# Kernel tuning notes

Measured on AMD Instinct MI355X. Metric: run time of the kernel, lower is better.

Reference implementation:

```python
import jax, jax.numpy as jnp
import numpy as np

GAMMA = 0.96875
HIDDEN = 512


def setup_inputs() -> dict:
    key = jax.random.key(0)
    kx, kq, kk, kv = jax.random.split(key, 4)
    B, S, H = 8, 2048, HIDDEN
    X = jax.random.normal(kx, (B, S, H), dtype=jnp.float32)
    # matches torch.randn(H, H) / H initialization
    W_Q = jax.random.normal(kq, (H, H), dtype=jnp.float32) / H
    W_K = jax.random.normal(kk, (H, H), dtype=jnp.float32) / H
    W_V = jax.random.normal(kv, (H, H), dtype=jnp.float32) / H  # v_dim == hidden (double_v_dim=False)
    return {"X": X, "W_Q": W_Q, "W_K": W_K, "W_V": W_V}


def reference(X, W_Q, W_K, W_V):
    # X: [B, S, H]
    Q = X @ W_Q  # [B, S, H]
    K = X @ W_K  # [B, S, H]
    V = X @ W_V  # [B, S, H]
    S_len = X.shape[1]
    idx = jnp.arange(S_len)
    D = GAMMA ** jnp.abs(idx[None, :] - idx[:, None]).astype(X.dtype)  # [S, S]
    scores = jnp.einsum('bsh,bth->bst', Q, K) * D  # [B, S, S]
    # swish(x) = x * sigmoid(x)
    ret = jnp.einsum('bst,bth->bsh', scores * jax.nn.sigmoid(scores), V)
    return ret
```

## Files before the change

### kernel.cpp

```cpp
#include <hip/hip_runtime.h>


typedef short  bf16x8 __attribute__((ext_vector_type(8)));
typedef float  f32x4  __attribute__((ext_vector_type(4)));

constexpr int S_LEN = 2048;
constexpr int HID   = 512;
constexpr int BAND  = 256;

#define GAMMA_L2 (-0.045803689613125f)
#define LOG2E    (1.4426950408889634f)

__device__ __forceinline__ ushort f2bf(float f) {
  union { float f; unsigned u; } v; v.f = f;
  unsigned u = v.u;
  u += 0x7FFFu + ((u >> 16) & 1u);
  return (ushort)(u >> 16);
}

__device__ __forceinline__ void gld_lds16(const ushort* g, ushort* l) {
  __builtin_amdgcn_global_load_lds(
      (const __attribute__((address_space(1))) void*)g,
      (__attribute__((address_space(3))) void*)l, 16, 0, 0);
}

__global__ void cvt_x_kernel(const float* __restrict__ X, ushort* __restrict__ Xb) {
  const int n4 = (8 * S_LEN * HID) / 4;
  int i = blockIdx.x * blockDim.x + threadIdx.x;
  const int stride = gridDim.x * blockDim.x;
  for (; i < n4; i += stride) {
    float4 v = ((const float4*)X)[i];
    ushort4 o;
    o.x = f2bf(v.x); o.y = f2bf(v.y); o.z = f2bf(v.z); o.w = f2bf(v.w);
    ((ushort4*)Xb)[i] = o;
  }
}

__global__ void cvt_w_kernel(const float* __restrict__ Wq, const float* __restrict__ Wk,
                             const float* __restrict__ Wv, ushort* __restrict__ Wtb) {
  __shared__ float tile[64][65];
  const int mat = blockIdx.z;
  const float* Wm = (mat == 0) ? Wq : ((mat == 1) ? Wk : Wv);
  const int k0 = blockIdx.y * 64, n0 = blockIdx.x * 64;
  const int t = threadIdx.x;
  const int c = t & 63, r0 = t >> 6;
  #pragma unroll
  for (int i = 0; i < 16; i++) {
    const int r = i * 4 + r0;
    tile[r][c] = Wm[(size_t)(k0 + r) * HID + n0 + c];
  }
  __syncthreads();
  ushort* Wt = Wtb + (size_t)mat * HID * HID;
  #pragma unroll
  for (int i = 0; i < 16; i++) {
    const int r = i * 4 + r0;
    Wt[(size_t)(n0 + r) * HID + k0 + c] = f2bf(tile[c][r]);
  }
}

__global__ void __launch_bounds__(256) proj_kernel(
    const ushort* __restrict__ Xb, const ushort* __restrict__ Wtb,
    ushort* __restrict__ Qb, ushort* __restrict__ Kb, ushort* __restrict__ Vtb) {
  __shared__ __align__(16) ushort lsA[2][128 * 64];
  __shared__ __align__(16) ushort lsB[2][128 * 64];
  const int bid  = blockIdx.x;
  const int xcd  = bid & 7;
  const int idx  = bid >> 3;
  const int rsub = idx / 12;
  const int cm   = idx - rsub * 12;
  const int mat  = cm >> 2;
  const int C0   = (cm & 3) * 128;
  const int R0   = (xcd * 16 + rsub) * 128;
  const int tid = threadIdx.x;
  const int w = tid >> 6, l = tid & 63;
  const int hl = l >> 4, l15 = l & 15;
  const int wr = w >> 1, wc = w & 1;
  const ushort* Wm = Wtb + (size_t)mat * HID * HID;

  const int srow = l >> 3;
  const int scol = ((l & 7) ^ srow) * 8;

  f32x4 acc[4][4] = {};

  #define STAGE_P(K0, BUF)                                                  \
    { _Pragma("unroll")                                                     \
      for (int j = 0; j < 4; j++) {                                         \
        const int i = w * 4 + j;                                            \
        const int r = i * 8 + srow;                                         \
        gld_lds16(Xb + (size_t)(R0 + r) * HID + (K0) + scol,                \
                  lsA[BUF] + i * 512);                                      \
        gld_lds16(Wm + (size_t)(C0 + r) * HID + (K0) + scol,                \
                  lsB[BUF] + i * 512);                                      \
      } }

  STAGE_P(0, 0);
  __syncthreads();

  #pragma unroll
  for (int it = 0; it < 8; it++) {
    const int cur = it & 1;
    if (it < 7) STAGE_P((it + 1) * 64, cur ^ 1);
    #pragma unroll
    for (int kf = 0; kf < 2; kf++) {
      bf16x8 af[4], bfr[4];
      #pragma unroll
      for (int mi = 0; mi < 4; mi++) {
        const int r  = wr * 64 + mi * 16 + l15;
        const int sl = ((kf * 4 + hl) ^ (r & 7)) * 8;
        af[mi] = *(const bf16x8*)(lsA[cur] + r * 64 + sl);
      }
      #pragma unroll
      for (int nj = 0; nj < 4; nj++) {
        const int r  = wc * 64 + nj * 16 + l15;
        const int sl = ((kf * 4 + hl) ^ (r & 7)) * 8;
        bfr[nj] = *(const bf16x8*)(lsB[cur] + r * 64 + sl);
      }
      #pragma unroll
      for (int mi = 0; mi < 4; mi++)
        #pragma unroll
        for (int nj = 0; nj < 4; nj++)
          acc[mi][nj] = __builtin_amdgcn_mfma_f32_16x16x32_bf16(
              af[mi], bfr[nj], acc[mi][nj], 0, 0, 0);
    }
    __syncthreads();
  }

  if (mat < 2) {
    ushort* Op = (mat == 0) ? Qb : Kb;
    #pragma unroll
    for (int mi = 0; mi < 4; mi++) {
      const int r16 = R0 + wr * 64 + mi * 16;
      const size_t sb = ((size_t)r16 >> 4) * 8192;
      #pragma unroll
      for (int nj = 0; nj < 4; nj++) {
        const int h = C0 + wc * 64 + nj * 16 + l15;
        const size_t ha = sb + (size_t)(h >> 3) * 128 + (h & 7);
        #pragma unroll
        for (int i = 0; i < 4; i++)
          Op[ha + (hl * 4 + i) * 8] = f2bf(acc[mi][nj][i]);
      }
    }
  } else {
    const int b = R0 >> 11;
    ushort* Vt = Vtb + (size_t)b * 1048576;
    #pragma unroll
    for (int mi = 0; mi < 4; mi++) {
      const int sb16 = (R0 & 2047) + wr * 64 + mi * 16;
      const size_t sa = (size_t)((sb16 >> 3) + (hl >> 1)) * 128 + (hl & 1) * 4;
      #pragma unroll
      for (int nj = 0; nj < 4; nj++) {
        const int hv = (C0 + wc * 64) / 16 + nj;
        ushort4 pk;
        pk.x = f2bf(acc[mi][nj][0]); pk.y = f2bf(acc[mi][nj][1]);
        pk.z = f2bf(acc[mi][nj][2]); pk.w = f2bf(acc[mi][nj][3]);
        *(ushort4*)(Vt + (size_t)hv * 32768 + sa + l15 * 8) = pk;
      }
    }
  }
}

__global__ void __launch_bounds__(256, 4) attn_kernel(
    const ushort* __restrict__ Q2, const ushort* __restrict__ K2,
    const ushort* __restrict__ V2, float* __restrict__ Out) {
  __shared__ __align__(16) ushort Qlds[16 * 512];
  __shared__ __align__(16) ushort Pb[2][16 * 72];
  const int b = blockIdx.x & 7, q0 = (blockIdx.x >> 3) * 16;
  const int tid = threadIdx.x;
  const int w = tid >> 6, l = tid & 63;
  const int hl = l >> 4, l15 = l & 15;

  const ushort* Qg = Q2 + ((size_t)(b * 128 + (q0 >> 4))) * 8192;
  #pragma unroll
  for (int j = 0; j < 4; j++) {
    const int kf = w * 4 + j;
    gld_lds16(Qg + kf * 512 + l * 8, Qlds + kf * 512);
  }

  f32x4 accO[8] = {};
  const int t_lo = (q0 - BAND) < 0 ? 0 : ((q0 - BAND) >> 6);
  int t_hi = ((q0 + 15 + BAND) >> 6) + 1;
  if (t_hi > S_LEN / 64) t_hi = S_LEN / 64;

  const float qrow = (float)(q0 + l15);
  const int bK = b * 128;
  const ushort* Vb = V2 + (size_t)b * 1048576 + (size_t)w * 8 * 32768
                        + hl * 128 + l15 * 8;

  #define QK_T(T, STV)                                                       \
    {                                                                        \
      const ushort* Kt = K2 + ((size_t)(bK + (T) * 4 + w)) * 8192 + l * 8;   \
      _Pragma("unroll")                                                      \
      for (int kf = 0; kf < 16; kf++) {                                      \
        bf16x8 kfr = *(const bf16x8*)(Kt + kf * 512);                        \
        bf16x8 qfr = *(const bf16x8*)(Qlds + kf * 512 + l * 8);              \
        STV = __builtin_amdgcn_mfma_f32_16x16x32_bf16(kfr, qfr, STV, 0, 0, 0); \
      }                                                                      \
    }

  #define SWISH_P(T, STV, BUF)                                               \
    {                                                                        \
      ushort4 pk;                                                            \
      _Pragma("unroll")                                                      \
      for (int i = 0; i < 4; i++) {                                          \
        const float kvf = (float)((T) * 64 + w * 16 + hl * 4 + i);           \
        const float ad = fabsf(kvf - qrow);                                  \
        const float s = STV[i] * exp2f(GAMMA_L2 * ad);                       \
        const float p = s * __builtin_amdgcn_rcpf(1.0f + exp2f(-LOG2E * s)); \
        ((ushort*)&pk)[i] = f2bf(p);                                         \
      }                                                                      \
      *(ushort4*)(Pb[BUF] + l15 * 72 + w * 16 + hl * 4) = pk;                \
    }

  #define PV_T(T, BUF)                                                       \
    {                                                                        \
      bf16x8 pa0 = *(const bf16x8*)(Pb[BUF] + l15 * 72 + hl * 8);            \
      bf16x8 pa1 = *(const bf16x8*)(Pb[BUF] + l15 * 72 + 32 + hl * 8);       \
      const ushort* Vt = Vb + (size_t)(T) * 1024;                            \
      _Pragma("unroll")                                                      \
      for (int nfi = 0; nfi < 8; nfi++) {                                    \
        bf16x8 v0 = *(const bf16x8*)(Vt + (size_t)nfi * 32768);              \
        bf16x8 v1 = *(const bf16x8*)(Vt + (size_t)nfi * 32768 + 512);        \
        accO[nfi] = __builtin_amdgcn_mfma_f32_16x16x32_bf16(pa0, v0, accO[nfi], 0, 0, 0); \
        accO[nfi] = __builtin_amdgcn_mfma_f32_16x16x32_bf16(pa1, v1, accO[nfi], 0, 0, 0); \
      }                                                                      \
    }

  __syncthreads();

  {
    f32x4 st = {};
    QK_T(t_lo, st);
    SWISH_P(t_lo, st, t_lo & 1);
  }
  __syncthreads();

  for (int t = t_lo; t < t_hi; ++t) {
    PV_T(t, t & 1);
    if (t + 1 < t_hi) {
      f32x4 st = {};
      QK_T(t + 1, st);
      SWISH_P(t + 1, st, (t + 1) & 1);
    }
    __syncthreads();
  }

  float* Ob = Out + ((size_t)b * S_LEN + q0) * HID + w * 128;
  #pragma unroll
  for (int nfi = 0; nfi < 8; nfi++)
    #pragma unroll
    for (int i = 0; i < 4; i++)
      Ob[(size_t)(hl * 4 + i) * HID + nfi * 16 + l15] = accO[nfi][i];
}

extern "C" void kernel_launch(void* const* d_in, const int* in_sizes, int n_in,
                              void* d_out, int out_size, void* d_ws, size_t ws_size,
                              hipStream_t stream) {
  const float* X  = (const float*)d_in[0];
  const float* Wq = (const float*)d_in[1];
  const float* Wk = (const float*)d_in[2];
  const float* Wv = (const float*)d_in[3];
  float* Out = (float*)d_out;

  char* ws = (char*)d_ws;
  ushort* Xb  = (ushort*)(ws);
  ushort* Wtb = (ushort*)(ws + 16777216);
  ushort* Qb  = (ushort*)(ws + 18350080);
  ushort* Kb  = (ushort*)(ws + 35127296);
  ushort* Vtb = (ushort*)(ws + 51904512);

  cvt_x_kernel<<<2048, 256, 0, stream>>>(X, Xb);
  cvt_w_kernel<<<dim3(8, 8, 3), 256, 0, stream>>>(Wq, Wk, Wv, Wtb);
  proj_kernel<<<1536, 256, 0, stream>>>(Xb, Wtb, Qb, Kb, Vtb);
  attn_kernel<<<1024, 256, 0, stream>>>(Qb, Kb, Vtb, Out);
}
```

Measured before the change: 181.5 us.

## Double proj waves per block and process two attention tiles per barrier

The projection kernel moves from 4 to 8 waves per 128x128 tile, so each wave computes a 64x32 sub-tile and stages fewer loads. The attention kernel now handles two key tiles per iteration with a 4-deep P buffer, which halves the number of block barriers. It also splits the QK accumulation into two independent MFMA chains to shorten the dependency latency. The costs are higher register and LDS pressure and a larger unrolled body, which may reduce occupancy.

```diff
diff --git a/kernel.cpp b/kernel.cpp
--- a/kernel.cpp
+++ b/kernel.cpp
@@ -58,7 +58,7 @@
   }
 }
 
-__global__ void __launch_bounds__(256) proj_kernel(
+__global__ void __launch_bounds__(512, 4) proj_kernel(
     const ushort* __restrict__ Xb, const ushort* __restrict__ Wtb,
     ushort* __restrict__ Qb, ushort* __restrict__ Kb, ushort* __restrict__ Vtb) {
   __shared__ __align__(16) ushort lsA[2][128 * 64];
@@ -74,18 +74,18 @@
   const int tid = threadIdx.x;
   const int w = tid >> 6, l = tid & 63;
   const int hl = l >> 4, l15 = l & 15;
-  const int wr = w >> 1, wc = w & 1;
+  const int wr = w >> 2, wc = w & 3;
   const ushort* Wm = Wtb + (size_t)mat * HID * HID;
 
   const int srow = l >> 3;
   const int scol = ((l & 7) ^ srow) * 8;
 
-  f32x4 acc[4][4] = {};
+  f32x4 acc[4][2] = {};
 
   #define STAGE_P(K0, BUF)                                                  \
     { _Pragma("unroll")                                                     \
-      for (int j = 0; j < 4; j++) {                                         \
-        const int i = w * 4 + j;                                            \
+      for (int j = 0; j < 2; j++) {                                         \
+        const int i = w * 2 + j;                                            \
         const int r = i * 8 + srow;                                         \
         gld_lds16(Xb + (size_t)(R0 + r) * HID + (K0) + scol,                \
                   lsA[BUF] + i * 512);                                      \
@@ -102,7 +102,7 @@
     if (it < 7) STAGE_P((it + 1) * 64, cur ^ 1);
     #pragma unroll
     for (int kf = 0; kf < 2; kf++) {
-      bf16x8 af[4], bfr[4];
+      bf16x8 af[4], bfr[2];
       #pragma unroll
       for (int mi = 0; mi < 4; mi++) {
         const int r  = wr * 64 + mi * 16 + l15;
@@ -110,15 +110,15 @@
         af[mi] = *(const bf16x8*)(lsA[cur] + r * 64 + sl);
       }
       #pragma unroll
-      for (int nj = 0; nj < 4; nj++) {
-        const int r  = wc * 64 + nj * 16 + l15;
+      for (int nj = 0; nj < 2; nj++) {
+        const int r  = wc * 32 + nj * 16 + l15;
         const int sl = ((kf * 4 + hl) ^ (r & 7)) * 8;
         bfr[nj] = *(const bf16x8*)(lsB[cur] + r * 64 + sl);
       }
       #pragma unroll
       for (int mi = 0; mi < 4; mi++)
         #pragma unroll
-        for (int nj = 0; nj < 4; nj++)
+        for (int nj = 0; nj < 2; nj++)
           acc[mi][nj] = __builtin_amdgcn_mfma_f32_16x16x32_bf16(
               af[mi], bfr[nj], acc[mi][nj], 0, 0, 0);
     }
@@ -132,8 +132,8 @@
       const int r16 = R0 + wr * 64 + mi * 16;
       const size_t sb = ((size_t)r16 >> 4) * 8192;
       #pragma unroll
-      for (int nj = 0; nj < 4; nj++) {
-        const int h = C0 + wc * 64 + nj * 16 + l15;
+      for (int nj = 0; nj < 2; nj++) {
+        const int h = C0 + wc * 32 + nj * 16 + l15;
         const size_t ha = sb + (size_t)(h >> 3) * 128 + (h & 7);
         #pragma unroll
         for (int i = 0; i < 4; i++)
@@ -148,8 +148,8 @@
       const int sb16 = (R0 & 2047) + wr * 64 + mi * 16;
       const size_t sa = (size_t)((sb16 >> 3) + (hl >> 1)) * 128 + (hl & 1) * 4;
       #pragma unroll
-      for (int nj = 0; nj < 4; nj++) {
-        const int hv = (C0 + wc * 64) / 16 + nj;
+      for (int nj = 0; nj < 2; nj++) {
+        const int hv = (C0 + wc * 32) / 16 + nj;
         ushort4 pk;
         pk.x = f2bf(acc[mi][nj][0]); pk.y = f2bf(acc[mi][nj][1]);
         pk.z = f2bf(acc[mi][nj][2]); pk.w = f2bf(acc[mi][nj][3]);
@@ -163,7 +163,7 @@
     const ushort* __restrict__ Q2, const ushort* __restrict__ K2,
     const ushort* __restrict__ V2, float* __restrict__ Out) {
   __shared__ __align__(16) ushort Qlds[16 * 512];
-  __shared__ __align__(16) ushort Pb[2][16 * 72];
+  __shared__ __align__(16) ushort Pb[4][16 * 72];
   const int b = blockIdx.x & 7, q0 = (blockIdx.x >> 3) * 16;
   const int tid = threadIdx.x;
   const int w = tid >> 6, l = tid & 63;
@@ -186,26 +186,32 @@
   const ushort* Vb = V2 + (size_t)b * 1048576 + (size_t)w * 8 * 32768
                         + hl * 128 + l15 * 8;
 
-  #define QK_T(T, STV)                                                       \
+  #define QK_T2(T, S0, S1)                                                   \
     {                                                                        \
       const ushort* Kt = K2 + ((size_t)(bK + (T) * 4 + w)) * 8192 + l * 8;   \
       _Pragma("unroll")                                                      \
-      for (int kf = 0; kf < 16; kf++) {                                      \
+      for (int kf = 0; kf < 8; kf++) {                                       \
         bf16x8 kfr = *(const bf16x8*)(Kt + kf * 512);                        \
         bf16x8 qfr = *(const bf16x8*)(Qlds + kf * 512 + l * 8);              \
-        STV = __builtin_amdgcn_mfma_f32_16x16x32_bf16(kfr, qfr, STV, 0, 0, 0); \
-      }                                                                      \
-    }
-
-  #define SWISH_P(T, STV, BUF)                                               \
+        S0 = __builtin_amdgcn_mfma_f32_16x16x32_bf16(kfr, qfr, S0, 0, 0, 0); \
+      }                                                                      \
+      _Pragma("unroll")                                                      \
+      for (int kf = 8; kf < 16; kf++) {                                      \
+        bf16x8 kfr = *(const bf16x8*)(Kt + kf * 512);                        \
+        bf16x8 qfr = *(const bf16x8*)(Qlds + kf * 512 + l * 8);              \
+        S1 = __builtin_amdgcn_mfma_f32_16x16x32_bf16(kfr, qfr, S1, 0, 0, 0); \
+      }                                                                      \
+    }
+
+  #define SWISH_P(T, S0, S1, BUF)                                            \
     {                                                                        \
       ushort4 pk;                                                            \
       _Pragma("unroll")                                                      \
       for (int i = 0; i < 4; i++) {                                          \
         const float kvf = (float)((T) * 64 + w * 16 + hl * 4 + i);           \
         const float ad = fabsf(kvf - qrow);                                  \
-        const float s = STV[i] * exp2f(GAMMA_L2 * ad);                       \
-        const float p = s * __builtin_amdgcn_rcpf(1.0f + exp2f(-LOG2E * s)); \
+        const float sv = (S0[i] + S1[i]) * exp2f(GAMMA_L2 * ad);             \
+        const float p = sv * __builtin_amdgcn_rcpf(1.0f + exp2f(-LOG2E * sv)); \
         ((ushort*)&pk)[i] = f2bf(p);                                         \
       }                                                                      \
       *(ushort4*)(Pb[BUF] + l15 * 72 + w * 16 + hl * 4) = pk;                \
@@ -228,18 +234,29 @@
   __syncthreads();
 
   {
-    f32x4 st = {};
-    QK_T(t_lo, st);
-    SWISH_P(t_lo, st, t_lo & 1);
-  }
-  __syncthreads();
-
-  for (int t = t_lo; t < t_hi; ++t) {
-    PV_T(t, t & 1);
-    if (t + 1 < t_hi) {
-      f32x4 st = {};
-      QK_T(t + 1, st);
-      SWISH_P(t + 1, st, (t + 1) & 1);
+    f32x4 s0 = {}, s1 = {};
+    QK_T2(t_lo, s0, s1);
+    SWISH_P(t_lo, s0, s1, t_lo & 3);
+  }
+  {
+    f32x4 s0 = {}, s1 = {};
+    QK_T2(t_lo + 1, s0, s1);
+    SWISH_P(t_lo + 1, s0, s1, (t_lo + 1) & 3);
+  }
+  __syncthreads();
+
+  for (int t = t_lo; t < t_hi; t += 2) {
+    PV_T(t, t & 3);
+    if (t + 1 < t_hi) PV_T(t + 1, (t + 1) & 3);
+    if (t + 2 < t_hi) {
+      f32x4 s0 = {}, s1 = {};
+      QK_T2(t + 2, s0, s1);
+      SWISH_P(t + 2, s0, s1, (t + 2) & 3);
+    }
+    if (t + 3 < t_hi) {
+      f32x4 s0 = {}, s1 = {};
+      QK_T2(t + 3, s0, s1);
+      SWISH_P(t + 3, s0, s1, (t + 3) & 3);
     }
     __syncthreads();
   }
@@ -270,6 +287,6 @@
 
   cvt_x_kernel<<<2048, 256, 0, stream>>>(X, Xb);
   cvt_w_kernel<<<dim3(8, 8, 3), 256, 0, stream>>>(Wq, Wk, Wv, Wtb);
-  proj_kernel<<<1536, 256, 0, stream>>>(Xb, Wtb, Qb, Kb, Vtb);
+  proj_kernel<<<1536, 512, 0, stream>>>(Xb, Wtb, Qb, Kb, Vtb);
   attn_kernel<<<1024, 256, 0, stream>>>(Qb, Kb, Vtb, Out);
 }
```

Result: faster. 172.0 us (-5.2%).
